# Performance work log

Measured on AMD Instinct MI355X. Metric: run time of the kernel, lower is better.

The kernel has to match this reference:

```python
import jax, jax.numpy as jnp
import numpy as np

T, N, E = 8, 20000, 320000
D_IN, H, OUT = 64, 128, 2
EPS = 1e-5  # BatchNorm eps


def setup_inputs() -> dict:
    key = jax.random.key(0)
    ks = jax.random.split(key, 24)
    rn = lambda k, shape: jax.random.normal(k, shape, jnp.float32) * 0.05
    inp = {
        "x_seq": jax.random.normal(ks[0], (T, N, D_IN), jnp.float32),
        "edge_index_seq": jax.random.randint(ks[1], (T, 2, E), 0, N),
        # GCN layer 1 (D_IN -> H) + BatchNorm (eval mode: running stats)
        "W1": rn(ks[2], (D_IN, H)), "b1": jnp.zeros((H,), jnp.float32),
        "g1": jnp.ones((H,), jnp.float32), "be1": jnp.zeros((H,), jnp.float32),
        "m1": rn(ks[3], (H,)), "v1": jax.random.uniform(ks[4], (H,), jnp.float32, 0.5, 1.5),
        # GCN layer 2 (H -> H) + BatchNorm
        "W2": rn(ks[5], (H, H)), "b2": jnp.zeros((H,), jnp.float32),
        "g2": jnp.ones((H,), jnp.float32), "be2": jnp.zeros((H,), jnp.float32),
        "m2": rn(ks[6], (H,)), "v2": jax.random.uniform(ks[7], (H,), jnp.float32, 0.5, 1.5),
        # LSTM layer 0 (PyTorch layout: W_ih [4H, in], W_hh [4H, H], gate order i,f,g,o)
        "Wih0": rn(ks[8], (4 * H, H)), "Whh0": rn(ks[9], (4 * H, H)),
        "bih0": jnp.zeros((4 * H,), jnp.float32), "bhh0": jnp.zeros((4 * H,), jnp.float32),
        # LSTM layer 1
        "Wih1": rn(ks[10], (4 * H, H)), "Whh1": rn(ks[11], (4 * H, H)),
        "bih1": jnp.zeros((4 * H,), jnp.float32), "bhh1": jnp.zeros((4 * H,), jnp.float32),
        # final classifier
        "Wc": rn(ks[12], (OUT, H)), "bc": jnp.zeros((OUT,), jnp.float32),
    }
    return inp


def gcn_conv(x, src, dst, W, b):
    # GCNConv: D^{-1/2}(A+I)D^{-1/2} X W + b, self-loops added
    n = x.shape[0]
    h = x @ W                                   # [N, F_out]
    loop = jnp.arange(n)
    s = jnp.concatenate([src, loop])
    d = jnp.concatenate([dst, loop])
    deg = jax.ops.segment_sum(jnp.ones(d.shape, x.dtype), d, num_segments=n)
    dinv = jax.lax.rsqrt(deg)                   # deg >= 1 (self-loops)
    coef = dinv[s] * dinv[d]                    # [E+N]
    agg = jax.ops.segment_sum(h[s] * coef[:, None], d, num_segments=n)
    return agg + b


def batchnorm_eval(x, g, b, m, v):
    return (x - m) * jax.lax.rsqrt(v + EPS) * g + b


def lstm_layer(xs, Wih, Whh, b):
    # xs: [T, in]; returns (ys [T,H], h_T [H])
    h0 = jnp.zeros((Whh.shape[1],), xs.dtype)

    def step(carry, xt):
        h, c = carry
        gates = xt @ Wih.T + h @ Whh.T + b
        i, f, g, o = jnp.split(gates, 4, axis=-1)
        c = jax.nn.sigmoid(f) * c + jax.nn.sigmoid(i) * jnp.tanh(g)
        h = jax.nn.sigmoid(o) * jnp.tanh(c)
        return (h, c), h

    (hT, _), ys = jax.lax.scan(step, (h0, h0), xs)
    return ys, hT


def reference(x_seq, edge_index_seq, W1, b1, g1, be1, m1, v1,
              W2, b2, g2, be2, m2, v2,
              Wih0, Whh0, bih0, bhh0, Wih1, Whh1, bih1, bhh1, Wc, bc):
    def per_t(x, e):
        src, dst = e[0], e[1]
        h = gcn_conv(x, src, dst, W1, b1)
        h = jax.nn.relu(batchnorm_eval(h, g1, be1, m1, v1))
        h = gcn_conv(h, src, dst, W2, b2)
        h = batchnorm_eval(h, g2, be2, m2, v2)
        return h.mean(axis=0)                   # global mean pool (batch=None)

    emb = jax.vmap(per_t)(x_seq, edge_index_seq)  # [T, H]
    ys, _ = lstm_layer(emb, Wih0, Whh0, bih0 + bhh0)
    _, hT = lstm_layer(ys, Wih1, Whh1, bih1 + bhh1)
    out = hT @ Wc.T + bc                          # [OUT]
    return (out[None, :], hT[None, :])
```

## Files before the change

### kernel.cpp

```cpp
#include <hip/hip_runtime.h>
#include <hip/hip_fp16.h>
#include <math.h>

#define T 8
#define N 20000
#define E 320000
#define EPS 1e-5f
#define NBA 32
#define CHUNKA 10000
#define NPACK 10000
#define NPACK4 5000
#define TILES_PT 1250
#define BW 625
#define NBUK 32
#define SPAN_MAX 13824

typedef _Float16 f16x8 __attribute__((ext_vector_type(8)));
typedef float f32x4 __attribute__((ext_vector_type(4)));

__device__ __forceinline__ float sigm(float x) { return 1.0f / (1.0f + expf(-x)); }

__global__ __launch_bounds__(256) void k_prepw(const float* __restrict__ W1,
                                               __half* __restrict__ W1t) {
    int i = blockIdx.x * 256 + threadIdx.x;
    if (i >= 64 * 128) return;
    int j = i & 127, k = i >> 7;
    W1t[j * 64 + k] = __float2half(W1[i]);
}

__global__ __launch_bounds__(1024) void k_partA(const int* __restrict__ edges,
                                                unsigned int* __restrict__ hist_g,
                                                unsigned int* __restrict__ bpart,
                                                int* __restrict__ bcnt) {
    __shared__ unsigned int arr[CHUNKA];
    __shared__ int cnt[NBUK], cur[NBUK];
    const int t = blockIdx.x & 7, b = blockIdx.x >> 3;
    const int tid = threadIdx.x;
    const int* keys = edges + (size_t)t * 2 * E + E + b * CHUNKA;
    const int* pays = edges + (size_t)t * 2 * E + b * CHUNKA;
    for (int i = tid; i < NPACK4; i += 1024) arr[i] = 0;
    if (tid < NBUK) cnt[tid] = 0;
    __syncthreads();
    for (int i = tid; i < CHUNKA; i += 1024) {
        int k = keys[i];
        atomicAdd(&arr[k >> 2], 1u << ((k & 3) * 8));
        atomicAdd(&cnt[k / BW], 1);
    }
    __syncthreads();
    unsigned int* hout = hist_g + (size_t)(t * NBA + b) * NPACK4;
    for (int i = tid; i < NPACK4; i += 1024) hout[i] = arr[i];
    if (tid == 0) {
        int run = 0;
        for (int u = 0; u < NBUK; u++) { cur[u] = run; run += cnt[u]; }
    }
    if (tid < NBUK) bcnt[(t * NBUK + tid) * NBUK + b] = cnt[tid];
    __syncthreads();
    for (int i = tid; i < CHUNKA; i += 1024) {
        int k = keys[i];
        int p = pays[i];
        int slot = atomicAdd(&cur[k / BW], 1);
        arr[slot] = ((unsigned int)k << 15) | (unsigned int)p;
    }
    __syncthreads();
    unsigned int* outp = bpart + (size_t)(t * NBUK + b) * CHUNKA;
    for (int i = tid; i < CHUNKA; i += 1024) outp[i] = arr[i];
}

__global__ __launch_bounds__(256) void k_colsum(
    const unsigned int* __restrict__ hist_g,
    int* __restrict__ dega, float* __restrict__ dinv) {
    int idx = blockIdx.x * 256 + threadIdx.x;
    if (idx >= T * NPACK4) return;
    int t = idx / NPACK4, i = idx - t * NPACK4;
    const unsigned int* hp = hist_g + (size_t)t * NBA * NPACK4 + i;
    unsigned int a0 = 0, a1 = 0, a2 = 0, a3 = 0;
#pragma unroll
    for (int b = 0; b < NBA; b++) {
        unsigned int h = hp[(size_t)b * NPACK4];
        a0 += h & 0xffu; a1 += (h >> 8) & 0xffu;
        a2 += (h >> 16) & 0xffu; a3 += h >> 24;
    }
    int4 dd; dd.x = (int)a0; dd.y = (int)a1; dd.z = (int)a2; dd.w = (int)a3;
    ((int4*)dega)[idx] = dd;
    float4 df;
    df.x = rsqrtf((float)a0 + 1.0f); df.y = rsqrtf((float)a1 + 1.0f);
    df.z = rsqrtf((float)a2 + 1.0f); df.w = rsqrtf((float)a3 + 1.0f);
    ((float4*)dinv)[idx] = df;
}

__global__ __launch_bounds__(1024) void k_scanN(const int* __restrict__ dega,
                                                int* __restrict__ offs) {
    const int t = blockIdx.x, tid = threadIdx.x;
    __shared__ int sh[1024];
    int local[20];
    int sum = 0;
    if (tid < 1000) {
        const int* tp = dega + t * N + tid * 20;
#pragma unroll
        for (int i = 0; i < 20; i++) { local[i] = tp[i]; sum += local[i]; }
    }
    sh[tid] = sum;
    __syncthreads();
    for (int off = 1; off < 1024; off <<= 1) {
        int v = (tid >= off) ? sh[tid - off] : 0;
        __syncthreads();
        sh[tid] += v;
        __syncthreads();
    }
    if (tid < 1000) {
        int run = t * E + sh[tid] - sum;
        int* op = offs + t * N + tid * 20;
#pragma unroll
        for (int i = 0; i < 20; i++) { op[i] = run; run += local[i]; }
    }
    if (t == T - 1 && tid == 0) offs[T * N] = T * E;
}

__global__ __launch_bounds__(256) void k_cvt(const float* __restrict__ x,
                                             const float* __restrict__ dinv,
                                             __half* __restrict__ xh) {
    int idx = blockIdx.x * 256 + threadIdx.x;
    if (idx >= T * N * 16) return;
    float d = dinv[idx >> 4];
    f32x4 vv = __builtin_nontemporal_load((const f32x4*)x + idx);
    __half h0 = __float2half(vv.x * d);
    __half h1 = __float2half(vv.y * d);
    __half h2 = __float2half(vv.z * d);
    __half h3 = __float2half(vv.w * d);
    ushort4 pack;
    pack.x = *(unsigned short*)&h0;
    pack.y = *(unsigned short*)&h1;
    pack.z = *(unsigned short*)&h2;
    pack.w = *(unsigned short*)&h3;
    ((ushort4*)xh)[idx] = pack;
}

__global__ __launch_bounds__(1024) void k_place(const unsigned int* __restrict__ bpart,
                                                const int* __restrict__ bcnt,
                                                const int* __restrict__ offs,
                                                int* __restrict__ eidx) {
    __shared__ int stage[SPAN_MAX];
    __shared__ int cursor[BW];
    __shared__ int offb[NBUK], lenb[NBUK];
    const int t = blockIdx.x & 7, u = blockIdx.x >> 3;
    const int tid = threadIdx.x;
    const int nodeBase = t * N + u * BW;
    const int dstBase = u * BW;
    const int segStart = offs[nodeBase];
    const int segEnd = offs[nodeBase + BW];
    const int span = segEnd - segStart;
    if (tid < NBUK) {
        int s = 0;
        for (int uu = 0; uu < u; uu++) s += bcnt[(t * NBUK + uu) * NBUK + tid];
        offb[tid] = s;
        lenb[tid] = bcnt[(t * NBUK + u) * NBUK + tid];
    }
    for (int j = tid; j < BW; j += 1024) cursor[j] = offs[nodeBase + j] - segStart;
    __syncthreads();
    if (span <= SPAN_MAX) {
        for (int b = 0; b < NBUK; b++) {
            const unsigned int* src = bpart + (size_t)(t * NBUK + b) * CHUNKA + offb[b];
            int len = lenb[b];
            for (int i = tid; i < len; i += 1024) {
                unsigned int it = src[i];
                int pos = atomicAdd(&cursor[(int)(it >> 15) - dstBase], 1);
                stage[pos] = (int)(it & 0x7fffu) << 5;
            }
            __syncthreads();
        }
        int* out = eidx + segStart;
        for (int i = tid; i < span; i += 1024) out[i] = stage[i];
    } else {
        for (int b = 0; b < NBUK; b++) {
            const unsigned int* src = bpart + (size_t)(t * NBUK + b) * CHUNKA + offb[b];
            int len = lenb[b];
            for (int i = tid; i < len; i += 1024) {
                unsigned int it = src[i];
                int pos = atomicAdd(&cursor[(int)(it >> 15) - dstBase], 1);
                eidx[segStart + pos] = (int)(it & 0x7fffu) << 5;
            }
            __syncthreads();
        }
    }
}

__global__ __launch_bounds__(1024) void k_wsum(const unsigned int* __restrict__ bpart,
                                               const float* __restrict__ dinv,
                                               float* __restrict__ wpart) {
    __shared__ float wf[NPACK];
    const int t = blockIdx.x & 7, b = blockIdx.x >> 3;
    const int tid = threadIdx.x;
    const unsigned int* run = bpart + (size_t)(t * NBUK + b) * CHUNKA;
    const float* dv = dinv + t * N;
    for (int half = 0; half < 2; half++) {
        for (int i = tid; i < NPACK; i += 1024) wf[i] = 0.f;
        __syncthreads();
        int lo = half * NPACK;
        for (int i = tid; i < CHUNKA; i += 1024) {
            unsigned int it = run[i];
            int q = (int)(it & 0x7fffu) - lo;
            if (q >= 0 && q < NPACK) atomicAdd(&wf[q], dv[it >> 15]);
        }
        __syncthreads();
        float* out = wpart + (size_t)(t * NBUK + b) * N + lo;
        for (int i = tid; i < NPACK; i += 1024) out[i] = wf[i];
        __syncthreads();
    }
}

__global__ __launch_bounds__(256) void k_wred(const float* __restrict__ wpart,
                                              const float* __restrict__ dinv,
                                              float* __restrict__ alpha) {
    int node = blockIdx.x * 256 + threadIdx.x;
    if (node >= T * N) return;
    int t = node / N, n = node - t * N;
    float s = 0.f;
#pragma unroll
    for (int b = 0; b < NBUK; b++) s += wpart[(size_t)(t * NBUK + b) * N + n];
    float di = dinv[node];
    alpha[node] = di * (s + di);
}

__global__ __launch_bounds__(256) void k_gather(
    const int* __restrict__ eidx, const int* __restrict__ offs,
    const float* __restrict__ dinv, const __half* __restrict__ xh,
    __half* __restrict__ vh) {
    const int t = blockIdx.x & 7;
    const int n = ((blockIdx.x >> 3) << 2) + (threadIdx.x >> 6);
    const int lane = threadIdx.x & 63;
    const int f = lane & 31, g = lane >> 5;
    if (n >= N) return;
    const int node = t * N + n;
    const int start = offs[node];
    const int end = offs[node + 1];
    const __half2* xt2 = (const __half2*)(xh + (size_t)t * N * 64);
    const int zrow = (T - t) * (N * 32);
    float acc0 = 0.f, acc1 = 0.f;
    for (int bs = start; bs < end; bs += 64) {
        int cnt = end - bs; if (cnt > 64) cnt = 64;
        int idx = zrow;
        if (lane < cnt) idx = __builtin_nontemporal_load(&eidx[bs + lane]);
        __half2 hacc = __float2half2_rn(0.f);
        for (int e = 0; e < cnt; e += 16) {
            int o0 = __shfl(idx, e + 0 + g),  o1 = __shfl(idx, e + 2 + g);
            int o2 = __shfl(idx, e + 4 + g),  o3 = __shfl(idx, e + 6 + g);
            int o4 = __shfl(idx, e + 8 + g),  o5 = __shfl(idx, e + 10 + g);
            int o6 = __shfl(idx, e + 12 + g), o7 = __shfl(idx, e + 14 + g);
            __half2 u0 = xt2[o0 + f], u1 = xt2[o1 + f];
            __half2 u2 = xt2[o2 + f], u3 = xt2[o3 + f];
            __half2 u4 = xt2[o4 + f], u5 = xt2[o5 + f];
            __half2 u6 = xt2[o6 + f], u7 = xt2[o7 + f];
            __half2 s01 = __hadd2(u0, u1), s23 = __hadd2(u2, u3);
            __half2 s45 = __hadd2(u4, u5), s67 = __hadd2(u6, u7);
            __half2 s03 = __hadd2(s01, s23), s47 = __hadd2(s45, s67);
            hacc = __hadd2(hacc, __hadd2(s03, s47));
        }
        float2 fa = __half22float2(hacc);
        acc0 += fa.x;
        acc1 += fa.y;
    }
    acc0 += __shfl_down(acc0, 32);
    acc1 += __shfl_down(acc1, 32);
    if (g == 0) {
        float di = dinv[node];
        float2 us = __half22float2(xt2[(n << 5) + f]);
        float r0 = di * (acc0 + us.x);
        float r1 = di * (acc1 + us.y);
        __half2 outp = __floats2half2_rn(r0, r1);
        ((__half2*)vh)[(size_t)node * 32 + f] = outp;
    }
}

__global__ __launch_bounds__(256) void k_mfma_pool(
    const __half* __restrict__ vh, const float* __restrict__ alpha,
    const __half* __restrict__ W1t,
    const float* __restrict__ b1, const float* __restrict__ g1,
    const float* __restrict__ be1, const float* __restrict__ m1,
    const float* __restrict__ v1, float* __restrict__ pooled) {
    const int t = blockIdx.x & 7;
    const int bt = blockIdx.x >> 3;
    const int w = threadIdx.x >> 6, lane = threadIdx.x & 63;
    const int q = lane >> 4, col = lane & 15;
    const size_t tb = (size_t)t * N;

    f16x8 bfr[8][2];
    float sbv[8], stv[8];
#pragma unroll
    for (int jt = 0; jt < 8; jt++) {
        int j = jt * 16 + col;
        float s = g1[j] * rsqrtf(v1[j] + EPS);
        sbv[jt] = s;
        stv[jt] = s * b1[j] + be1[j] - m1[j] * s;
#pragma unroll
        for (int kk = 0; kk < 2; kk++)
            bfr[jt][kk] = *(const f16x8*)(W1t + (size_t)j * 64 + kk * 32 + q * 8);
    }
    float pool8[8];
#pragma unroll
    for (int jt = 0; jt < 8; jt++) pool8[jt] = 0.f;

    for (int i = 0; i < 8; i++) {
        int tau = bt * 32 + w * 8 + i;
        if (tau >= TILES_PT) break;
        int nb = tau * 16;
        const __half* vrow = vh + (tb + nb + col) * 64;
        f16x8 a0 = *(const f16x8*)(vrow + q * 8);
        f16x8 a1 = *(const f16x8*)(vrow + 32 + q * 8);
        float4 af = ((const float4*)(alpha + tb + nb))[q];
#pragma unroll
        for (int jt = 0; jt < 8; jt++) {
            f32x4 acc = {0.f, 0.f, 0.f, 0.f};
            acc = __builtin_amdgcn_mfma_f32_16x16x32_f16(a0, bfr[jt][0], acc, 0, 0, 0);
            acc = __builtin_amdgcn_mfma_f32_16x16x32_f16(a1, bfr[jt][1], acc, 0, 0, 0);
            float s = sbv[jt], sh = stv[jt];
            pool8[jt] += fmaxf(s * acc[0] + sh, 0.f) * af.x
                       + fmaxf(s * acc[1] + sh, 0.f) * af.y
                       + fmaxf(s * acc[2] + sh, 0.f) * af.z
                       + fmaxf(s * acc[3] + sh, 0.f) * af.w;
        }
    }
#pragma unroll
    for (int jt = 0; jt < 8; jt++) {
        pool8[jt] += __shfl_xor(pool8[jt], 16);
        pool8[jt] += __shfl_xor(pool8[jt], 32);
    }
    if (lane < 16) {
#pragma unroll
        for (int jt = 0; jt < 8; jt++)
            atomicAdd(&pooled[t * 128 + jt * 16 + lane], pool8[jt]);
    }
}

__global__ __launch_bounds__(256) void k_warm(const float* __restrict__ a,
                                              const float* __restrict__ b,
                                              const float* __restrict__ c,
                                              float* __restrict__ sink) {
    int slice = blockIdx.x >> 3;
    int start = slice * 24576;
    float s = 0.f;
    for (int i = start + threadIdx.x; i < start + 24576; i += 256) {
        float v;
        if (i < 65536) v = a[i];
        else if (i < 131072) v = b[i - 65536];
        else v = c[i - 131072];
        s += v;
    }
    sink[blockIdx.x * 256 + threadIdx.x] = s;
}

__global__ __launch_bounds__(512) void k_emb(
    const float* __restrict__ pooled,
    const float* __restrict__ W2, const float* __restrict__ b2,
    const float* __restrict__ g2, const float* __restrict__ be2,
    const float* __restrict__ m2, const float* __restrict__ v2,
    const float* __restrict__ Wih0, const float* __restrict__ bih0,
    const float* __restrict__ bhh0, float* __restrict__ gx0_g) {
    const int t = blockIdx.x, tid = threadIdx.x;
    __shared__ float pm[128];
    __shared__ float es[128];
    if (tid < 128) pm[tid] = pooled[t * 128 + tid] * (1.0f / N);
    __syncthreads();
    if (tid < 128) {
        float s = g2[tid] * rsqrtf(v2[tid] + EPS);
        float sh = be2[tid] - m2[tid] * s;
        float dot = 0.f;
#pragma unroll 8
        for (int k = 0; k < 128; k++) dot += pm[k] * W2[k * 128 + tid];
        es[tid] = s * (dot + b2[tid]) + sh;
    }
    __syncthreads();
    float dot = bih0[tid] + bhh0[tid];
    const float4* w = (const float4*)(Wih0 + tid * 128);
    const float4* e4 = (const float4*)es;
#pragma unroll
    for (int k4 = 0; k4 < 32; k4++) {
        float4 a = w[k4], bb = e4[k4];
        dot += a.x * bb.x + a.y * bb.y + a.z * bb.z + a.w * bb.w;
    }
    gx0_g[t * 512 + tid] = dot;
}

__global__ __launch_bounds__(1024) void k_head(
    const float* __restrict__ gx0_g,
    const float* __restrict__ Whh0, const float* __restrict__ Whh1,
    const float* __restrict__ Wih1, const float* __restrict__ bih1,
    const float* __restrict__ bhh1,
    const float* __restrict__ Wc, const float* __restrict__ bc,
    float* __restrict__ out) {
    __shared__ float gx0[T][512];
    __shared__ float gx1h[2][T][512];
    __shared__ float ys[T][128];
    __shared__ float h[128];
    __shared__ float part[1024];
    const int tid = threadIdx.x;
    const int r = tid & 511, hf = tid >> 9;

    for (int i = tid; i < T * 512; i += 1024) gx0[i >> 9][i & 511] = gx0_g[i];
    if (tid < 128) h[tid] = 0.f;
    float c = 0.f;
    __syncthreads();

    {
        const float4* wrow = (const float4*)(Whh0 + r * 128 + hf * 64);
        for (int t = 0; t < T; t++) {
            const float4* h4 = ((const float4*)h) + hf * 16;
            float dot = 0.f;
#pragma unroll
            for (int k = 0; k < 16; k++) {
                float4 wv = wrow[k];
                float4 hv = h4[k];
                dot += wv.x * hv.x + wv.y * hv.y + wv.z * hv.z + wv.w * hv.w;
            }
            part[tid] = dot;
            __syncthreads();
            if (tid < 128) {
                float i_ = gx0[t][tid]       + part[tid]       + part[512 + tid];
                float f_ = gx0[t][128 + tid] + part[128 + tid] + part[640 + tid];
                float g_ = gx0[t][256 + tid] + part[256 + tid] + part[768 + tid];
                float o_ = gx0[t][384 + tid] + part[384 + tid] + part[896 + tid];
                c = sigm(f_) * c + sigm(i_) * tanhf(g_);
                float hv = sigm(o_) * tanhf(c);
                h[tid] = hv;
                ys[t][tid] = hv;
            }
            __syncthreads();
        }
    }

    {
        const float4* wrow = (const float4*)(Wih1 + r * 128 + hf * 64);
        float bias = (hf == 0) ? (bih1[r] + bhh1[r]) : 0.f;
        for (int t = 0; t < T; t++) {
            const float4* y4 = ((const float4*)ys[t]) + hf * 16;
            float dot = bias;
#pragma unroll
            for (int k = 0; k < 16; k++) {
                float4 wv = wrow[k];
                float4 yv = y4[k];
                dot += wv.x * yv.x + wv.y * yv.y + wv.z * yv.z + wv.w * yv.w;
            }
            gx1h[hf][t][r] = dot;
        }
    }

    if (tid < 128) h[tid] = 0.f;
    c = 0.f;
    __syncthreads();
    {
        const float4* wrow = (const float4*)(Whh1 + r * 128 + hf * 64);
        for (int t = 0; t < T; t++) {
            const float4* h4 = ((const float4*)h) + hf * 16;
            float dot = 0.f;
#pragma unroll
            for (int k = 0; k < 16; k++) {
                float4 wv = wrow[k];
                float4 hv = h4[k];
                dot += wv.x * hv.x + wv.y * hv.y + wv.z * hv.z + wv.w * hv.w;
            }
            part[tid] = dot;
            __syncthreads();
            if (tid < 128) {
                float i_ = gx1h[0][t][tid]       + gx1h[1][t][tid]       + part[tid]       + part[512 + tid];
                float f_ = gx1h[0][t][128 + tid] + gx1h[1][t][128 + tid] + part[128 + tid] + part[640 + tid];
                float g_ = gx1h[0][t][256 + tid] + gx1h[1][t][256 + tid] + part[256 + tid] + part[768 + tid];
                float o_ = gx1h[0][t][384 + tid] + gx1h[1][t][384 + tid] + part[384 + tid] + part[896 + tid];
                c = sigm(f_) * c + sigm(i_) * tanhf(g_);
                h[tid] = sigm(o_) * tanhf(c);
            }
            __syncthreads();
        }
    }

    if (tid < 2) {
        float dot = bc[tid];
#pragma unroll 8
        for (int k = 0; k < 128; k++) dot += h[k] * Wc[tid * 128 + k];
        out[tid] = dot;
    }
    if (tid < 128) out[2 + tid] = h[tid];
}

extern "C" void kernel_launch(void* const* d_in, const int* in_sizes, int n_in,
                              void* d_out, int out_size, void* d_ws, size_t ws_size,
                              hipStream_t stream) {
    const float* x    = (const float*)d_in[0];
    const int*   edges= (const int*)d_in[1];
    const float* W1   = (const float*)d_in[2];
    const float* b1   = (const float*)d_in[3];
    const float* g1   = (const float*)d_in[4];
    const float* be1  = (const float*)d_in[5];
    const float* m1   = (const float*)d_in[6];
    const float* v1   = (const float*)d_in[7];
    const float* W2   = (const float*)d_in[8];
    const float* b2   = (const float*)d_in[9];
    const float* g2   = (const float*)d_in[10];
    const float* be2  = (const float*)d_in[11];
    const float* m2   = (const float*)d_in[12];
    const float* v2   = (const float*)d_in[13];
    const float* Wih0 = (const float*)d_in[14];
    const float* Whh0 = (const float*)d_in[15];
    const float* bih0 = (const float*)d_in[16];
    const float* bhh0 = (const float*)d_in[17];
    const float* Wih1 = (const float*)d_in[18];
    const float* Whh1 = (const float*)d_in[19];
    const float* bih1 = (const float*)d_in[20];
    const float* bhh1 = (const float*)d_in[21];
    const float* Wc   = (const float*)d_in[22];
    const float* bc   = (const float*)d_in[23];

    char* base = (char*)d_ws;
    unsigned int* hist_g = (unsigned int*)base;
    unsigned int* bpart  = (unsigned int*)(base + (size_t)T * NBA * NPACK * 4);
    __half*       vh     = (__half*)base;
    char* p = base + (size_t)T * NBA * NPACK * 4 + (size_t)T * NBUK * CHUNKA * 4;
    __half* xh   = (__half*)p;              p += (size_t)T * N * 64 * 2 + 128;
    int*   offs  = (int*)p;                 p += (size_t)(T * N + 1) * 4 + 12;
    int*   dega  = (int*)p;                 p += (size_t)T * N * 4;
    float* dinv  = (float*)p;               p += (size_t)T * N * 4;
    float* alpha = (float*)p;               p += (size_t)T * N * 4;
    int*   tot   = (int*)p;                 p += (size_t)T * N * 4;
    int*   eidx  = (int*)p;                 p += (size_t)T * E * 4;
    float* wpart = (float*)p;               p += (size_t)T * NBUK * N * 4;
    int*   bcnt  = (int*)p;                 p += (size_t)T * NBUK * NBUK * 4;
    float* pooled= (float*)p;               p += (size_t)T * 128 * 4;
    float* gx0_g = (float*)p;               p += (size_t)T * 512 * 4;
    __half* W1t  = (__half*)p;

    (void)hipMemsetAsync(pooled, 0, T * 128 * sizeof(float), stream);
    (void)hipMemsetAsync(xh + (size_t)T * N * 64, 0, 128, stream);

    k_prepw<<<32, 256, 0, stream>>>(W1, W1t);
    k_partA<<<T * NBUK, 1024, 0, stream>>>(edges, hist_g, bpart, bcnt);
    k_colsum<<<(T * NPACK4 + 255) / 256, 256, 0, stream>>>(hist_g, dega, dinv);
    k_scanN<<<T, 1024, 0, stream>>>(dega, offs);
    k_place<<<T * NBUK, 1024, 0, stream>>>(bpart, bcnt, offs, eidx);
    k_wsum<<<T * NBUK, 1024, 0, stream>>>(bpart, dinv, wpart);
    k_wred<<<(T * N + 255) / 256, 256, 0, stream>>>(wpart, dinv, alpha);
    k_cvt<<<(T * N * 16 + 255) / 256, 256, 0, stream>>>(x, dinv, xh);
    k_gather<<<(T * N) / 4, 256, 0, stream>>>(eidx, offs, dinv, xh, vh);
    k_mfma_pool<<<8 * 40, 256, 0, stream>>>(vh, alpha, W1t, b1, g1, be1, m1, v1, pooled);

    k_warm<<<64, 256, 0, stream>>>(Whh0, Whh1, Wih1, (float*)tot);
    k_emb<<<T, 512, 0, stream>>>(pooled, W2, b2, g2, be2, m2, v2, Wih0, bih0, bhh0, gx0_g);
    k_head<<<1, 1024, 0, stream>>>(gx0_g, Whh0, Whh1, Wih1, bih1, bhh1, Wc, bc, (float*)d_out);
}
```

Baseline: 371.6 us.

## Merge small kernels and memsets to cut launches; split LSTM head with register weights

Folds the W1 transpose and the pooled zeroing into k_colsum as extra blocks, merges the alpha reduction and the xh pad zeroing into k_cvt, and folds the L2 warm-up pass into k_emb as extra blocks. The two hipMemsetAsync calls go away. The single LSTM head kernel is split into k_lstm0 and k_lstm1, each holding its weight slice in registers rather than reloading it every step, with ys handed over through global memory. The aim is fewer launches and serial gaps, at the cost of one extra launch for the LSTM split, higher register pressure, and a warm-up that now runs alongside the embedding blocks instead of before them.

```diff
diff --git a/kernel.cpp b/kernel.cpp
--- a/kernel.cpp
+++ b/kernel.cpp
@@ -14,19 +14,12 @@
 #define BW 625
 #define NBUK 32
 #define SPAN_MAX 13824
+#define CSGRID 157
 
 typedef _Float16 f16x8 __attribute__((ext_vector_type(8)));
 typedef float f32x4 __attribute__((ext_vector_type(4)));
 
 __device__ __forceinline__ float sigm(float x) { return 1.0f / (1.0f + expf(-x)); }
-
-__global__ __launch_bounds__(256) void k_prepw(const float* __restrict__ W1,
-                                               __half* __restrict__ W1t) {
-    int i = blockIdx.x * 256 + threadIdx.x;
-    if (i >= 64 * 128) return;
-    int j = i & 127, k = i >> 7;
-    W1t[j * 64 + k] = __float2half(W1[i]);
-}
 
 __global__ __launch_bounds__(1024) void k_partA(const int* __restrict__ edges,
                                                 unsigned int* __restrict__ hist_g,
@@ -68,8 +61,21 @@
 
 __global__ __launch_bounds__(256) void k_colsum(
     const unsigned int* __restrict__ hist_g,
-    int* __restrict__ dega, float* __restrict__ dinv) {
-    int idx = blockIdx.x * 256 + threadIdx.x;
+    int* __restrict__ dega, float* __restrict__ dinv,
+    const float* __restrict__ W1, __half* __restrict__ W1t,
+    float* __restrict__ pooled) {
+    const int bid = blockIdx.x, tid = threadIdx.x;
+    if (bid >= CSGRID) {
+        int i = (bid - CSGRID) * 256 + tid;
+        int j = i & 127, k = i >> 7;
+        W1t[j * 64 + k] = __float2half(W1[i]);
+        if (bid == CSGRID) {
+            f32x4 z = {0.f, 0.f, 0.f, 0.f};
+            ((f32x4*)pooled)[tid] = z;
+        }
+        return;
+    }
+    int idx = bid * 256 + tid;
     if (idx >= T * NPACK4) return;
     int t = idx / NPACK4, i = idx - t * NPACK4;
     const unsigned int* hp = hist_g + (size_t)t * NBA * NPACK4 + i;
@@ -114,25 +120,6 @@
         for (int i = 0; i < 20; i++) { op[i] = run; run += local[i]; }
     }
     if (t == T - 1 && tid == 0) offs[T * N] = T * E;
-}
-
-__global__ __launch_bounds__(256) void k_cvt(const float* __restrict__ x,
-                                             const float* __restrict__ dinv,
-                                             __half* __restrict__ xh) {
-    int idx = blockIdx.x * 256 + threadIdx.x;
-    if (idx >= T * N * 16) return;
-    float d = dinv[idx >> 4];
-    f32x4 vv = __builtin_nontemporal_load((const f32x4*)x + idx);
-    __half h0 = __float2half(vv.x * d);
-    __half h1 = __float2half(vv.y * d);
-    __half h2 = __float2half(vv.z * d);
-    __half h3 = __float2half(vv.w * d);
-    ushort4 pack;
-    pack.x = *(unsigned short*)&h0;
-    pack.y = *(unsigned short*)&h1;
-    pack.z = *(unsigned short*)&h2;
-    pack.w = *(unsigned short*)&h3;
-    ((ushort4*)xh)[idx] = pack;
 }
 
 __global__ __launch_bounds__(1024) void k_place(const unsigned int* __restrict__ bpart,
@@ -208,17 +195,37 @@
     }
 }
 
-__global__ __launch_bounds__(256) void k_wred(const float* __restrict__ wpart,
-                                              const float* __restrict__ dinv,
-                                              float* __restrict__ alpha) {
-    int node = blockIdx.x * 256 + threadIdx.x;
-    if (node >= T * N) return;
-    int t = node / N, n = node - t * N;
-    float s = 0.f;
-#pragma unroll
-    for (int b = 0; b < NBUK; b++) s += wpart[(size_t)(t * NBUK + b) * N + n];
-    float di = dinv[node];
-    alpha[node] = di * (s + di);
+__global__ __launch_bounds__(256) void k_cvt(const float* __restrict__ x,
+                                             const float* __restrict__ dinv,
+                                             const float* __restrict__ wpart,
+                                             float* __restrict__ alpha,
+                                             __half* __restrict__ xh) {
+    int idx = blockIdx.x * 256 + threadIdx.x;
+    if (idx >= T * N * 16) return;
+    if (idx < T * N) {
+        int t = idx / N, n = idx - t * N;
+        float s = 0.f;
+#pragma unroll
+        for (int b = 0; b < NBUK; b++) s += wpart[(size_t)(t * NBUK + b) * N + n];
+        float di = dinv[idx];
+        alpha[idx] = di * (s + di);
+    }
+    if (idx < 16) {
+        ushort4 z; z.x = 0; z.y = 0; z.z = 0; z.w = 0;
+        ((ushort4*)(xh + (size_t)T * N * 64))[idx] = z;
+    }
+    float d = dinv[idx >> 4];
+    f32x4 vv = __builtin_nontemporal_load((const f32x4*)x + idx);
+    __half h0 = __float2half(vv.x * d);
+    __half h1 = __float2half(vv.y * d);
+    __half h2 = __float2half(vv.z * d);
+    __half h3 = __float2half(vv.w * d);
+    ushort4 pack;
+    pack.x = *(unsigned short*)&h0;
+    pack.y = *(unsigned short*)&h1;
+    pack.z = *(unsigned short*)&h2;
+    pack.w = *(unsigned short*)&h3;
+    ((ushort4*)xh)[idx] = pack;
 }
 
 __global__ __launch_bounds__(256) void k_gather(
@@ -331,31 +338,31 @@
     }
 }
 
-__global__ __launch_bounds__(256) void k_warm(const float* __restrict__ a,
-                                              const float* __restrict__ b,
-                                              const float* __restrict__ c,
-                                              float* __restrict__ sink) {
-    int slice = blockIdx.x >> 3;
-    int start = slice * 24576;
-    float s = 0.f;
-    for (int i = start + threadIdx.x; i < start + 24576; i += 256) {
-        float v;
-        if (i < 65536) v = a[i];
-        else if (i < 131072) v = b[i - 65536];
-        else v = c[i - 131072];
-        s += v;
-    }
-    sink[blockIdx.x * 256 + threadIdx.x] = s;
-}
-
 __global__ __launch_bounds__(512) void k_emb(
     const float* __restrict__ pooled,
     const float* __restrict__ W2, const float* __restrict__ b2,
     const float* __restrict__ g2, const float* __restrict__ be2,
     const float* __restrict__ m2, const float* __restrict__ v2,
     const float* __restrict__ Wih0, const float* __restrict__ bih0,
-    const float* __restrict__ bhh0, float* __restrict__ gx0_g) {
-    const int t = blockIdx.x, tid = threadIdx.x;
+    const float* __restrict__ bhh0, float* __restrict__ gx0_g,
+    const float* __restrict__ Whh0, const float* __restrict__ Whh1,
+    const float* __restrict__ Wih1, float* __restrict__ sink) {
+    const int tid = threadIdx.x;
+    if (blockIdx.x >= T) {
+        int bid = blockIdx.x - T;
+        int start = (bid >> 3) * 24576;
+        float s = 0.f;
+        for (int i = start + tid; i < start + 24576; i += 512) {
+            float v;
+            if (i < 65536) v = Whh0[i];
+            else if (i < 131072) v = Whh1[i - 65536];
+            else v = Wih1[i - 131072];
+            s += v;
+        }
+        sink[bid * 512 + tid] = s;
+        return;
+    }
+    const int t = blockIdx.x;
     __shared__ float pm[128];
     __shared__ float es[128];
     if (tid < 128) pm[tid] = pooled[t * 128 + tid] * (1.0f / N);
@@ -380,97 +387,112 @@
     gx0_g[t * 512 + tid] = dot;
 }
 
-__global__ __launch_bounds__(1024) void k_head(
-    const float* __restrict__ gx0_g,
-    const float* __restrict__ Whh0, const float* __restrict__ Whh1,
-    const float* __restrict__ Wih1, const float* __restrict__ bih1,
-    const float* __restrict__ bhh1,
-    const float* __restrict__ Wc, const float* __restrict__ bc,
-    float* __restrict__ out) {
+__global__ __launch_bounds__(1024) void k_lstm0(
+    const float* __restrict__ gx0_g, const float* __restrict__ Whh0,
+    float* __restrict__ ys_g) {
     __shared__ float gx0[T][512];
-    __shared__ float gx1h[2][T][512];
-    __shared__ float ys[T][128];
     __shared__ float h[128];
     __shared__ float part[1024];
     const int tid = threadIdx.x;
     const int r = tid & 511, hf = tid >> 9;
-
+    float4 wreg[16];
+    {
+        const float4* wrow = (const float4*)(Whh0 + r * 128 + hf * 64);
+#pragma unroll
+        for (int k = 0; k < 16; k++) wreg[k] = wrow[k];
+    }
     for (int i = tid; i < T * 512; i += 1024) gx0[i >> 9][i & 511] = gx0_g[i];
     if (tid < 128) h[tid] = 0.f;
     float c = 0.f;
     __syncthreads();
-
-    {
-        const float4* wrow = (const float4*)(Whh0 + r * 128 + hf * 64);
-        for (int t = 0; t < T; t++) {
-            const float4* h4 = ((const float4*)h) + hf * 16;
-            float dot = 0.f;
-#pragma unroll
-            for (int k = 0; k < 16; k++) {
-                float4 wv = wrow[k];
-                float4 hv = h4[k];
-                dot += wv.x * hv.x + wv.y * hv.y + wv.z * hv.z + wv.w * hv.w;
-            }
-            part[tid] = dot;
-            __syncthreads();
-            if (tid < 128) {
-                float i_ = gx0[t][tid]       + part[tid]       + part[512 + tid];
-                float f_ = gx0[t][128 + tid] + part[128 + tid] + part[640 + tid];
-                float g_ = gx0[t][256 + tid] + part[256 + tid] + part[768 + tid];
-                float o_ = gx0[t][384 + tid] + part[384 + tid] + part[896 + tid];
-                c = sigm(f_) * c + sigm(i_) * tanhf(g_);
-                float hv = sigm(o_) * tanhf(c);
-                h[tid] = hv;
-                ys[t][tid] = hv;
-            }
-            __syncthreads();
-        }
-    }
-
+    for (int t = 0; t < T; t++) {
+        const float4* h4 = ((const float4*)h) + hf * 16;
+        float dot = 0.f;
+#pragma unroll
+        for (int k = 0; k < 16; k++) {
+            float4 wv = wreg[k];
+            float4 hv = h4[k];
+            dot += wv.x * hv.x + wv.y * hv.y + wv.z * hv.z + wv.w * hv.w;
+        }
+        part[tid] = dot;
+        __syncthreads();
+        if (tid < 128) {
+            float i_ = gx0[t][tid]       + part[tid]       + part[512 + tid];
+            float f_ = gx0[t][128 + tid] + part[128 + tid] + part[640 + tid];
+            float g_ = gx0[t][256 + tid] + part[256 + tid] + part[768 + tid];
+            float o_ = gx0[t][384 + tid] + part[384 + tid] + part[896 + tid];
+            c = sigm(f_) * c + sigm(i_) * tanhf(g_);
+            float hv = sigm(o_) * tanhf(c);
+            h[tid] = hv;
+            ys_g[t * 128 + tid] = hv;
+        }
+        __syncthreads();
+    }
+}
+
+__global__ __launch_bounds__(1024) void k_lstm1(
+    const float* __restrict__ ys_g,
+    const float* __restrict__ Wih1, const float* __restrict__ bih1,
+    const float* __restrict__ bhh1, const float* __restrict__ Whh1,
+    const float* __restrict__ Wc, const float* __restrict__ bc,
+    float* __restrict__ out) {
+    __shared__ float ys[T][128];
+    __shared__ float gx1h[2][T][512];
+    __shared__ float h[128];
+    __shared__ float part[1024];
+    const int tid = threadIdx.x;
+    const int r = tid & 511, hf = tid >> 9;
+    float4 wreg[16];
     {
         const float4* wrow = (const float4*)(Wih1 + r * 128 + hf * 64);
+#pragma unroll
+        for (int k = 0; k < 16; k++) wreg[k] = wrow[k];
+    }
+    for (int i = tid; i < T * 128; i += 1024) ys[i >> 7][i & 127] = ys_g[i];
+    __syncthreads();
+    {
         float bias = (hf == 0) ? (bih1[r] + bhh1[r]) : 0.f;
         for (int t = 0; t < T; t++) {
             const float4* y4 = ((const float4*)ys[t]) + hf * 16;
             float dot = bias;
 #pragma unroll
             for (int k = 0; k < 16; k++) {
-                float4 wv = wrow[k];
+                float4 wv = wreg[k];
                 float4 yv = y4[k];
                 dot += wv.x * yv.x + wv.y * yv.y + wv.z * yv.z + wv.w * yv.w;
             }
             gx1h[hf][t][r] = dot;
         }
     }
-
-    if (tid < 128) h[tid] = 0.f;
-    c = 0.f;
-    __syncthreads();
     {
         const float4* wrow = (const float4*)(Whh1 + r * 128 + hf * 64);
-        for (int t = 0; t < T; t++) {
-            const float4* h4 = ((const float4*)h) + hf * 16;
-            float dot = 0.f;
-#pragma unroll
-            for (int k = 0; k < 16; k++) {
-                float4 wv = wrow[k];
-                float4 hv = h4[k];
-                dot += wv.x * hv.x + wv.y * hv.y + wv.z * hv.z + wv.w * hv.w;
-            }
-            part[tid] = dot;
-            __syncthreads();
-            if (tid < 128) {
-                float i_ = gx1h[0][t][tid]       + gx1h[1][t][tid]       + part[tid]       + part[512 + tid];
-                float f_ = gx1h[0][t][128 + tid] + gx1h[1][t][128 + tid] + part[128 + tid] + part[640 + tid];
-                float g_ = gx1h[0][t][256 + tid] + gx1h[1][t][256 + tid] + part[256 + tid] + part[768 + tid];
-                float o_ = gx1h[0][t][384 + tid] + gx1h[1][t][384 + tid] + part[384 + tid] + part[896 + tid];
-                c = sigm(f_) * c + sigm(i_) * tanhf(g_);
-                h[tid] = sigm(o_) * tanhf(c);
-            }
-            __syncthreads();
-        }
-    }
-
+#pragma unroll
+        for (int k = 0; k < 16; k++) wreg[k] = wrow[k];
+    }
+    if (tid < 128) h[tid] = 0.f;
+    float c = 0.f;
+    __syncthreads();
+    for (int t = 0; t < T; t++) {
+        const float4* h4 = ((const float4*)h) + hf * 16;
+        float dot = 0.f;
+#pragma unroll
+        for (int k = 0; k < 16; k++) {
+            float4 wv = wreg[k];
+            float4 hv = h4[k];
+            dot += wv.x * hv.x + wv.y * hv.y + wv.z * hv.z + wv.w * hv.w;
+        }
+        part[tid] = dot;
+        __syncthreads();
+        if (tid < 128) {
+            float i_ = gx1h[0][t][tid]       + gx1h[1][t][tid]       + part[tid]       + part[512 + tid];
+            float f_ = gx1h[0][t][128 + tid] + gx1h[1][t][128 + tid] + part[128 + tid] + part[640 + tid];
+            float g_ = gx1h[0][t][256 + tid] + gx1h[1][t][256 + tid] + part[256 + tid] + part[768 + tid];
+            float o_ = gx1h[0][t][384 + tid] + gx1h[1][t][384 + tid] + part[384 + tid] + part[896 + tid];
+            c = sigm(f_) * c + sigm(i_) * tanhf(g_);
+            h[tid] = sigm(o_) * tanhf(c);
+        }
+        __syncthreads();
+    }
     if (tid < 2) {
         float dot = bc[tid];
 #pragma unroll 8
@@ -524,23 +546,19 @@
     int*   bcnt  = (int*)p;                 p += (size_t)T * NBUK * NBUK * 4;
     float* pooled= (float*)p;               p += (size_t)T * 128 * 4;
     float* gx0_g = (float*)p;               p += (size_t)T * 512 * 4;
+    float* ys_g  = (float*)p;               p += (size_t)T * 128 * 4;
     __half* W1t  = (__half*)p;
 
-    (void)hipMemsetAsync(pooled, 0, T * 128 * sizeof(float), stream);
-    (void)hipMemsetAsync(xh + (size_t)T * N * 64, 0, 128, stream);
-
-    k_prepw<<<32, 256, 0, stream>>>(W1, W1t);
     k_partA<<<T * NBUK, 1024, 0, stream>>>(edges, hist_g, bpart, bcnt);
-    k_colsum<<<(T * NPACK4 + 255) / 256, 256, 0, stream>>>(hist_g, dega, dinv);
+    k_colsum<<<CSGRID + 32, 256, 0, stream>>>(hist_g, dega, dinv, W1, W1t, pooled);
     k_scanN<<<T, 1024, 0, stream>>>(dega, offs);
     k_place<<<T * NBUK, 1024, 0, stream>>>(bpart, bcnt, offs, eidx);
     k_wsum<<<T * NBUK, 1024, 0, stream>>>(bpart, dinv, wpart);
-    k_wred<<<(T * N + 255) / 256, 256, 0, stream>>>(wpart, dinv, alpha);
-    k_cvt<<<(T * N * 16 + 255) / 256, 256, 0, stream>>>(x, dinv, xh);
+    k_cvt<<<(T * N * 16) / 256, 256, 0, stream>>>(x, dinv, wpart, alpha, xh);
     k_gather<<<(T * N) / 4, 256, 0, stream>>>(eidx, offs, dinv, xh, vh);
     k_mfma_pool<<<8 * 40, 256, 0, stream>>>(vh, alpha, W1t, b1, g1, be1, m1, v1, pooled);
-
-    k_warm<<<64, 256, 0, stream>>>(Whh0, Whh1, Wih1, (float*)tot);
-    k_emb<<<T, 512, 0, stream>>>(pooled, W2, b2, g2, be2, m2, v2, Wih0, bih0, bhh0, gx0_g);
-    k_head<<<1, 1024, 0, stream>>>(gx0_g, Whh0, Whh1, Wih1, bih1, bhh1, Wc, bc, (float*)d_out);
-}
+    k_emb<<<T + 64, 512, 0, stream>>>(pooled, W2, b2, g2, be2, m2, v2, Wih0, bih0, bhh0,
+                                      gx0_g, Whh0, Whh1, Wih1, (float*)tot);
+    k_lstm0<<<1, 1024, 0, stream>>>(gx0_g, Whh0, ys_g);
+    k_lstm1<<<1, 1024, 0, stream>>>(ys_g, Wih1, bih1, bhh1, Whh1, Wc, bc, (float*)d_out);
+}
```

New measurement: 335.3 us. 9.8% less time.
